# Kernel optimization log

Hardware: AMD Instinct MI355X
Metric: run time of the kernel (lower is better)

The kernel has to match this reference:

```python
import jax, jax.numpy as jnp
import numpy as np

STRIDE = 4
VOX = float(STRIDE + 1)  # voxel_size = [stride+1, stride+1]
IMG_W, IMG_H = 640.0, 480.0
N, F, E, FE, B = 300000, 64, 2400000, 8, 8


def setup_inputs() -> dict:
    key = jax.random.key(0)
    ks = jax.random.split(key, 6)
    x = jax.random.normal(ks[0], (N, F), jnp.float32)
    t = jax.random.uniform(ks[1], (N, 1), jnp.float32) * 100.0
    xy = jax.random.uniform(ks[2], (N, 2), jnp.float32) * jnp.array([IMG_W, IMG_H], jnp.float32)
    pos = jnp.concatenate([t, xy], axis=1)  # [N,3] = (time, x, y)
    batch = jnp.sort(jax.random.randint(ks[3], (N,), 0, B, jnp.int32))
    edge_index = jax.random.randint(ks[4], (2, E), 0, N, jnp.int32)
    edge_attr = jax.random.normal(ks[5], (E, FE), jnp.float32)
    return {"x": x, "pos": pos, "batch": batch, "edge_index": edge_index, "edge_attr": edge_attr}


def _forward(x, pos, batch, edge_index, edge_attr):
    n = x.shape[0]
    e = edge_index.shape[1]
    # ---- voxel_grid on pos[:,1:3] with per-sample batch separation ----
    p = pos[:, 1:3]
    start = jnp.min(p, axis=0)
    end = jnp.max(p, axis=0)
    coords = jnp.floor((p - start) / VOX).astype(jnp.int32)            # [N,2]
    dims = (jnp.floor((end - start) / VOX) + 1.0).astype(jnp.int32)    # [2]
    raw = batch * (dims[0] * dims[1]) + coords[:, 0] * dims[1] + coords[:, 1]
    # ---- consecutive_cluster: relabel voxel ids to 0..C-1 ----
    fill = jnp.iinfo(jnp.int32).max
    uniq, cluster = jnp.unique(raw, return_inverse=True, size=n, fill_value=fill)
    n_clusters = jnp.sum(uniq != fill)
    # ---- node pooling: scatter-max x, scatter-mean pos, batch per cluster ----
    new_x = jax.ops.segment_max(x, cluster, num_segments=n)
    cnt = jax.ops.segment_sum(jnp.ones((n,), pos.dtype), cluster, num_segments=n)
    new_pos = jax.ops.segment_sum(pos, cluster, num_segments=n) / jnp.maximum(cnt, 1.0)[:, None]
    new_batch = jax.ops.segment_max(batch, cluster, num_segments=n)
    valid = jnp.arange(n) < n_clusters
    new_x = jnp.where(valid[:, None], new_x, 0.0)
    new_pos = jnp.where(valid[:, None], new_pos, 0.0)
    new_batch = jnp.where(valid, new_batch, -1)
    # pos[:,1:3] //= scale (float floor-division, as torch // on float tensors)
    new_pos = new_pos.at[:, 1:3].set(jnp.floor(new_pos[:, 1:3] / float(STRIDE)))
    # ---- pool_edge: remap to cluster ids, drop self-loops, coalesce (sum attr) ----
    cs = cluster[edge_index[0]]
    cd = cluster[edge_index[1]]
    loop = cs == cd
    cs = jnp.where(loop, n, cs)   # sentinel group for self-loops (sorts last)
    cd = jnp.where(loop, n, cd)
    order = jnp.lexsort((cd, cs))
    cs_s, cd_s, ea_s = cs[order], cd[order], edge_attr[order]
    newg = jnp.concatenate([jnp.ones((1,), bool), (cs_s[1:] != cs_s[:-1]) | (cd_s[1:] != cd_s[:-1])])
    gid = jnp.cumsum(newg.astype(jnp.int32)) - 1
    src = jax.ops.segment_max(cs_s, gid, num_segments=e)
    dst = jax.ops.segment_max(cd_s, gid, num_segments=e)
    new_ea = jax.ops.segment_sum(ea_s, gid, num_segments=e)
    evalid = (jnp.arange(e) <= gid[-1]) & (src >= 0) & (src < n)
    new_edge_index = jnp.stack([jnp.where(evalid, src, -1), jnp.where(evalid, dst, -1)])
    new_ea = jnp.where(evalid[:, None], new_ea, 0.0)
    return new_x, new_pos, new_batch, new_edge_index, new_ea


def reference(x, pos, batch, edge_index, edge_attr):
    return _forward(x, pos, batch, edge_index, edge_attr)
```

## Files before the change

kernel.cpp:

```cpp
#include <hip/hip_runtime.h>

#define NN 300000
#define FF 64
#define EE 2400000
#define FEA 8
#define RAWCAP 131072
#define NCS 131072
#define NBUCK 2048
#define NSB 512
#define TILE ((EE + NSB - 1) / NSB)
#define CAP 4096

typedef unsigned long long ull;

__device__ __forceinline__ unsigned fenc(float f) {
  unsigned b = __float_as_uint(f);
  return (b & 0x80000000u) ? ~b : (b | 0x80000000u);
}
__device__ __forceinline__ float fdec(unsigned e) {
  unsigned b = (e & 0x80000000u) ? (e ^ 0x80000000u) : ~e;
  return __uint_as_float(b);
}

__global__ void init_hdr_k(unsigned* hdr) {
  if (threadIdx.x == 0) {
    hdr[0] = 0xFFFFFFFFu; hdr[1] = 0xFFFFFFFFu;
    hdr[2] = 0u;          hdr[3] = 0u;
  }
}

__global__ void minmax_k(const float* __restrict__ pos, unsigned* hdr) {
  __shared__ unsigned red[4][4];
  int t = blockIdx.x * blockDim.x + threadIdx.x;
  float mnx = 1e30f, mny = 1e30f, mxx = -1e30f, mxy = -1e30f;
  for (int i = t; i < NN; i += gridDim.x * blockDim.x) {
    float px = pos[i * 3 + 1], py = pos[i * 3 + 2];
    mnx = fminf(mnx, px); mny = fminf(mny, py);
    mxx = fmaxf(mxx, px); mxy = fmaxf(mxy, py);
  }
  for (int o = 1; o < 64; o <<= 1) {
    mnx = fminf(mnx, __shfl_xor(mnx, o));
    mny = fminf(mny, __shfl_xor(mny, o));
    mxx = fmaxf(mxx, __shfl_xor(mxx, o));
    mxy = fmaxf(mxy, __shfl_xor(mxy, o));
  }
  int wid = threadIdx.x >> 6;
  if ((threadIdx.x & 63) == 0) {
    red[wid][0] = fenc(mnx); red[wid][1] = fenc(mny);
    red[wid][2] = fenc(mxx); red[wid][3] = fenc(mxy);
  }
  __syncthreads();
  if (threadIdx.x == 0) {
    unsigned a0 = red[0][0], a1 = red[0][1], a2 = red[0][2], a3 = red[0][3];
    for (int k = 1; k < 4; k++) {
      a0 = min(a0, red[k][0]); a1 = min(a1, red[k][1]);
      a2 = max(a2, red[k][2]); a3 = max(a3, red[k][3]);
    }
    atomicMin(&hdr[0], a0); atomicMin(&hdr[1], a1);
    atomicMax(&hdr[2], a2); atomicMax(&hdr[3], a3);
  }
}

__global__ void dims_k(unsigned* hdr) {
  if (threadIdx.x == 0 && blockIdx.x == 0) {
    float mnx = fdec(hdr[0]), mny = fdec(hdr[1]);
    float mxx = fdec(hdr[2]), mxy = fdec(hdr[3]);
    int d0 = (int)(floorf((mxx - mnx) / 5.0f) + 1.0f);
    int d1 = (int)(floorf((mxy - mny) / 5.0f) + 1.0f);
    hdr[4] = (unsigned)d0;
    hdr[5] = (unsigned)d1;
    ((float*)hdr)[6] = mnx;
    ((float*)hdr)[7] = mny;
  }
}

__global__ void raw_k(const float* __restrict__ pos, const int* __restrict__ batch,
                      const unsigned* __restrict__ hdr, int* __restrict__ cluster,
                      unsigned* __restrict__ flags) {
  int i = blockIdx.x * blockDim.x + threadIdx.x;
  if (i >= NN) return;
  float mnx = ((const float*)hdr)[6], mny = ((const float*)hdr)[7];
  int d0 = (int)hdr[4], d1 = (int)hdr[5];
  int c0 = (int)floorf((pos[i * 3 + 1] - mnx) / 5.0f);
  int c1 = (int)floorf((pos[i * 3 + 2] - mny) / 5.0f);
  int raw = batch[i] * (d0 * d1) + c0 * d1 + c1;
  cluster[i] = raw;
  flags[raw] = 1u;
}

__global__ void __launch_bounds__(256)
scan_lb_k(const unsigned* __restrict__ in, unsigned* __restrict__ out, int ntot,
          unsigned* __restrict__ total_out, ull* __restrict__ desc, int nb) {
  __shared__ unsigned sc[256];
  __shared__ unsigned s_pref;
  int bid = blockIdx.x;
  int base = bid * 1024 + threadIdx.x * 4;
  unsigned v[4]; unsigned s = 0;
#pragma unroll
  for (int k = 0; k < 4; k++) {
    int i = base + k;
    v[k] = (i < ntot) ? in[i] : 0u;
    s += v[k];
  }
  sc[threadIdx.x] = s;
  __syncthreads();
  unsigned xv = s;
  for (int o = 1; o < 256; o <<= 1) {
    unsigned y = (threadIdx.x >= o) ? sc[threadIdx.x - o] : 0u;
    __syncthreads();
    xv += y;
    sc[threadIdx.x] = xv;
    __syncthreads();
  }
  unsigned btot = sc[255];
  if (threadIdx.x == 0) {
    unsigned ex = 0;
    if (bid == 0) {
      atomicExch(&desc[0], (2ULL << 32) | (ull)btot);
    } else {
      atomicExch(&desc[bid], (1ULL << 32) | (ull)btot);
      int p = bid - 1;
      while (true) {
        ull d = atomicAdd(&desc[p], 0ULL);
        unsigned fl = (unsigned)(d >> 32);
        if (fl == 2u) { ex += (unsigned)d; break; }
        if (fl == 1u) { ex += (unsigned)d; --p; }
      }
      atomicExch(&desc[bid], (2ULL << 32) | (ull)(ex + btot));
    }
    s_pref = ex;
    if (total_out && bid == nb - 1) *total_out = ex + btot;
  }
  __syncthreads();
  unsigned run = s_pref + xv - s;
#pragma unroll
  for (int k = 0; k < 4; k++) {
    int i = base + k;
    if (i < ntot) out[i] = run;
    run += v[k];
  }
}

__global__ void node_cnt_k(const unsigned* __restrict__ rank, int* __restrict__ cluster,
                           unsigned* __restrict__ cnt) {
  int i = blockIdx.x * blockDim.x + threadIdx.x;
  if (i >= NN) return;
  unsigned cl = rank[cluster[i]];
  unsigned r = atomicAdd(&cnt[cl], 1u);
  cluster[i] = (int)((r << 17) | cl);
}

__global__ void node_scatter_k(const int* __restrict__ cluster,
                               const unsigned* __restrict__ node_off,
                               int* __restrict__ nlist) {
  int i = blockIdx.x * blockDim.x + threadIdx.x;
  if (i >= NN) return;
  unsigned c = (unsigned)cluster[i];
  nlist[node_off[c & 0x1FFFFu] + (c >> 17)] = i;
}

__global__ void __launch_bounds__(256)
cluster_reduce_k(const float* __restrict__ x, const float* __restrict__ pos,
                 const int* __restrict__ batch, const int* __restrict__ nlist,
                 const unsigned* __restrict__ node_off, const unsigned* __restrict__ hdr,
                 float* __restrict__ out_x, float* __restrict__ out_pos,
                 float* __restrict__ out_batch) {
  int w = (blockIdx.x * blockDim.x + threadIdx.x) >> 6;
  int nw = (gridDim.x * blockDim.x) >> 6;
  int f = threadIdx.x & 63;
  int ncl = (int)hdr[8];
  for (int c = w; c < ncl; c += nw) {
    unsigned o0 = node_off[c];
    int len = (int)(node_off[c + 1] - o0);
    float mx = -1e38f;
    long long ps = 0;
    for (int m = 0; m < len; m++) {
      int nd = nlist[o0 + m];
      mx = fmaxf(mx, x[(size_t)nd * FF + f]);
      if (f < 3) ps += (long long)llrintf(pos[nd * 3 + f] * 65536.0f);
    }
    out_x[(size_t)c * FF + f] = mx;
    if (f < 3) {
      float v = (float)((double)ps / 65536.0 / (double)len);
      if (f > 0) v = floorf(v / 4.0f);
      out_pos[c * 3 + f] = v;
    }
    if (f == 63) out_batch[c] = (float)batch[nlist[o0]];
  }
}

__global__ void node_tail_k(const unsigned* __restrict__ hdr,
                            float* __restrict__ out_x, float* __restrict__ out_pos,
                            float* __restrict__ out_batch) {
  int ncl = (int)hdr[8];
  int total = (NN - ncl) * FF;
  for (int i = blockIdx.x * blockDim.x + threadIdx.x; i < total;
       i += gridDim.x * blockDim.x) {
    int r = ncl + (i >> 6), f = i & 63;
    out_x[(size_t)r * FF + f] = 0.0f;
    if (f < 3) out_pos[r * 3 + f] = 0.0f;
    if (f == 0) out_batch[r] = -1.0f;
  }
}


__global__ void __launch_bounds__(256)
coarse_cnt_k(const int* __restrict__ ei, const int* __restrict__ cluster,
             unsigned* __restrict__ mat) {
  __shared__ unsigned h[NBUCK];
  for (int i = threadIdx.x; i < NBUCK; i += 256) h[i] = 0u;
  __syncthreads();
  int t0 = blockIdx.x * TILE;
  for (int k = threadIdx.x; k < TILE; k += 256) {
    int t = t0 + k;
    if (t >= EE) break;
    unsigned s = (unsigned)cluster[ei[t]] & 0x1FFFFu;
    unsigned d = (unsigned)cluster[ei[EE + t]] & 0x1FFFFu;
    if (s != d) atomicAdd(&h[s >> 6], 1u);
  }
  __syncthreads();
  for (int i = threadIdx.x; i < NBUCK; i += 256)
    mat[(size_t)blockIdx.x * NBUCK + i] = h[i];
}

__global__ void transpose_k(const unsigned* __restrict__ mat, unsigned* __restrict__ matT) {
  int f = blockIdx.x * blockDim.x + threadIdx.x;
  if (f >= NSB * NBUCK) return;
  int cb = f / NSB, blk = f - cb * NSB;
  matT[f] = mat[(size_t)blk * NBUCK + cb];
}

__global__ void __launch_bounds__(256)
coarse_scatter_k(const int* __restrict__ ei, const int* __restrict__ cluster,
                 const unsigned* __restrict__ matT, ull* __restrict__ keys) {
  __shared__ unsigned cur[NBUCK];
  for (int i = threadIdx.x; i < NBUCK; i += 256)
    cur[i] = matT[(size_t)i * NSB + blockIdx.x];
  __syncthreads();
  int t0 = blockIdx.x * TILE;
  for (int k = threadIdx.x; k < TILE; k += 256) {
    int t = t0 + k;
    if (t >= EE) break;
    unsigned s = (unsigned)cluster[ei[t]] & 0x1FFFFu;
    unsigned d = (unsigned)cluster[ei[EE + t]] & 0x1FFFFu;
    if (s == d) continue;
    unsigned p = atomicAdd(&cur[s >> 6], 1u);
    keys[p] = ((ull)(s & 63u) << 39) | ((ull)d << 22) | (unsigned)t;
  }
}

__global__ void __launch_bounds__(256)
grp_emit_k(const ull* __restrict__ keys, const unsigned* __restrict__ matT,
           unsigned* __restrict__ hdr, ull* __restrict__ desc,
           const float* __restrict__ ea,
           float* __restrict__ out_src, float* __restrict__ out_dst,
           float* __restrict__ out_ea) {
  __shared__ ull sk2[CAP];
  __shared__ unsigned char hflag[CAP];
  __shared__ unsigned h[64], pre[65], cur[64], hc[64], hpre[64];
  __shared__ unsigned sG, sBase, sCnt;
  int cb = blockIdx.x;
  int tid = threadIdx.x;
  unsigned start = matT[(size_t)cb * NSB];
  unsigned end = (cb == NBUCK - 1) ? hdr[11] : matT[(size_t)(cb + 1) * NSB];
  int len = (int)(end - start);
  bool lds = (len <= CAP);
  unsigned G = 0;

  if (len > 0 && lds) {
    if (tid < 64) h[tid] = 0u;
    __syncthreads();
    for (int i = tid; i < len; i += 256)
      atomicAdd(&h[(unsigned)(keys[start + i] >> 39) & 63u], 1u);
    __syncthreads();
    if (tid == 0) {
      unsigned run = 0;
      for (int j = 0; j < 64; j++) { pre[j] = run; run += h[j]; }
      pre[64] = run;
    }
    __syncthreads();
    if (tid < 64) cur[tid] = pre[tid];
    __syncthreads();
    for (int i = tid; i < len; i += 256) {
      ull v = keys[start + i];
      unsigned j = (unsigned)(v >> 39) & 63u;
      sk2[atomicAdd(&cur[j], 1u)] = v;
    }
    __syncthreads();
    for (int i = tid; i < len; i += 256) {
      ull v = sk2[i];
      unsigned j = (unsigned)(v >> 39) & 63u;
      unsigned key23 = (unsigned)(v >> 22);
      bool head = true;
      for (int q = (int)pre[j]; q < i; ++q)
        if ((unsigned)(sk2[q] >> 22) == key23) { head = false; break; }
      hflag[i] = head ? 1 : 0;
    }
    __syncthreads();
    if (tid < 64) {
      unsigned c = 0;
      for (unsigned q = pre[tid]; q < pre[tid + 1]; ++q) c += hflag[q];
      hc[tid] = c;
    }
    __syncthreads();
    if (tid == 0) {
      unsigned run = 0;
      for (int j = 0; j < 64; j++) { hpre[j] = run; run += hc[j]; }
      sG = run;
    }
    __syncthreads();
    G = sG;
  } else if (len > 0) {
    if (tid == 0) sG = 0;
    __syncthreads();
    for (int j = 0; j < 64; j++) {
      if (tid == 0) sCnt = 0;
      __syncthreads();
      for (int i = tid; i < len; i += 256) {
        ull v = keys[start + i];
        if (((unsigned)(v >> 39) & 63u) == (unsigned)j) {
          unsigned p = atomicAdd(&sCnt, 1u);
          if (p < CAP) sk2[p] = v;
        }
      }
      __syncthreads();
      int sl = min((int)sCnt, CAP);
      for (int i = tid; i < sl; i += 256) {
        unsigned key23 = (unsigned)(sk2[i] >> 22);
        bool head = true;
        for (int q = 0; q < i; ++q)
          if ((unsigned)(sk2[q] >> 22) == key23) { head = false; break; }
        hflag[i] = head ? 1 : 0;
      }
      __syncthreads();
      if (tid == 0) {
        unsigned c = 0;
        for (int q = 0; q < sl; ++q) c += hflag[q];
        hc[j] = c; hpre[j] = sG; sG += c;
      }
      __syncthreads();
    }
    G = sG;
  }

  if (tid == 0) {
    unsigned ex = 0;
    if (cb == 0) {
      atomicExch(&desc[0], (2ULL << 32) | (ull)G);
    } else {
      atomicExch(&desc[cb], (1ULL << 32) | (ull)G);
      int p = cb - 1;
      while (true) {
        ull d = atomicAdd(&desc[p], 0ULL);
        unsigned fl = (unsigned)(d >> 32);
        if (fl == 2u) { ex += (unsigned)d; break; }
        if (fl == 1u) { ex += (unsigned)d; --p; }
      }
      atomicExch(&desc[cb], (2ULL << 32) | (ull)(ex + G));
    }
    sBase = ex;
    if (cb == NBUCK - 1) hdr[12] = ex + G;
  }
  __syncthreads();
  unsigned base = sBase;
  if (len <= 0) return;

  if (lds) {
    for (int i = tid; i < len; i += 256) {
      if (!hflag[i]) continue;
      ull v = sk2[i];
      unsigned j = (unsigned)(v >> 39) & 63u;
      unsigned key23 = (unsigned)(v >> 22);
      unsigned r = 0;
      for (unsigned q = pre[j]; q < pre[j + 1]; ++q)
        if (hflag[q] && (unsigned)(sk2[q] >> 22) < key23) r++;
      unsigned eid = (unsigned)(v & 0x3FFFFFULL);
      const float4* p4 = (const float4*)&ea[(size_t)eid * FEA];
      float4 a0 = p4[0], a1 = p4[1];
      bool single = (hc[j] == pre[j + 1] - pre[j]);
      if (!single) {
        for (unsigned q = pre[j]; q < pre[j + 1]; ++q) {
          if (q == (unsigned)i) continue;
          ull v2 = sk2[q];
          if ((unsigned)(v2 >> 22) == key23) {
            const float4* q4 = (const float4*)&ea[(size_t)(v2 & 0x3FFFFFULL) * FEA];
            float4 b0 = q4[0], b1 = q4[1];
            a0.x += b0.x; a0.y += b0.y; a0.z += b0.z; a0.w += b0.w;
            a1.x += b1.x; a1.y += b1.y; a1.z += b1.z; a1.w += b1.w;
          }
        }
      }
      unsigned row = base + hpre[j] + r;
      out_src[row] = (float)(cb * 64 + (int)j);
      out_dst[row] = (float)(key23 & 0x1FFFFu);
      float4* o = (float4*)&out_ea[(size_t)row * FEA];
      o[0] = a0; o[1] = a1;
    }
  } else {
    for (int j = 0; j < 64; j++) {
      if (tid == 0) sCnt = 0;
      __syncthreads();
      for (int i = tid; i < len; i += 256) {
        ull v = keys[start + i];
        if (((unsigned)(v >> 39) & 63u) == (unsigned)j) {
          unsigned p = atomicAdd(&sCnt, 1u);
          if (p < CAP) sk2[p] = v;
        }
      }
      __syncthreads();
      int sl = min((int)sCnt, CAP);
      for (int i = tid; i < sl; i += 256) {
        unsigned key23 = (unsigned)(sk2[i] >> 22);
        bool head = true;
        for (int q = 0; q < i; ++q)
          if ((unsigned)(sk2[q] >> 22) == key23) { head = false; break; }
        hflag[i] = head ? 1 : 0;
      }
      __syncthreads();
      for (int i = tid; i < sl; i += 256) {
        if (!hflag[i]) continue;
        ull v = sk2[i];
        unsigned key23 = (unsigned)(v >> 22);
        unsigned r = 0;
        for (int q = 0; q < sl; ++q)
          if (hflag[q] && (unsigned)(sk2[q] >> 22) < key23) r++;
        const float4* p4 = (const float4*)&ea[(size_t)(v & 0x3FFFFFULL) * FEA];
        float4 a0 = p4[0], a1 = p4[1];
        bool single = (hc[j] == (unsigned)sl);
        if (!single) {
          for (int q = 0; q < sl; ++q) {
            if (q == i) continue;
            ull v2 = sk2[q];
            if ((unsigned)(v2 >> 22) == key23) {
              const float4* q4 = (const float4*)&ea[(size_t)(v2 & 0x3FFFFFULL) * FEA];
              float4 b0 = q4[0], b1 = q4[1];
              a0.x += b0.x; a0.y += b0.y; a0.z += b0.z; a0.w += b0.w;
              a1.x += b1.x; a1.y += b1.y; a1.z += b1.z; a1.w += b1.w;
            }
          }
        }
        unsigned row = base + hpre[j] + r;
        out_src[row] = (float)(cb * 64 + j);
        out_dst[row] = (float)(key23 & 0x1FFFFu);
        float4* o = (float4*)&out_ea[(size_t)row * FEA];
        o[0] = a0; o[1] = a1;
      }
      __syncthreads();
    }
  }
}

__global__ void tail_fill_k(const unsigned* __restrict__ hdr,
                            float* __restrict__ out_src, float* __restrict__ out_dst,
                            float* __restrict__ out_ea) {
  int T = (int)hdr[12];
  for (int t = T + blockIdx.x * blockDim.x + threadIdx.x; t < EE;
       t += gridDim.x * blockDim.x) {
    out_src[t] = -1.0f;
    out_dst[t] = -1.0f;
    float4 z = make_float4(0.f, 0.f, 0.f, 0.f);
    float4* o = (float4*)&out_ea[(size_t)t * FEA];
    o[0] = z; o[1] = z;
  }
}

extern "C" void kernel_launch(void* const* d_in, const int* in_sizes, int n_in,
                              void* d_out, int out_size, void* d_ws, size_t ws_size,
                              hipStream_t stream) {
  const float* x   = (const float*)d_in[0];
  const float* pos = (const float*)d_in[1];
  const int* batch = (const int*)d_in[2];
  const int* ei    = (const int*)d_in[3];
  const float* ea  = (const float*)d_in[4];
  float* out = (float*)d_out;

  const size_t OX = 0;
  const size_t OP = (size_t)NN * FF;
  const size_t OB = OP + (size_t)NN * 3;
  const size_t OE = OB + (size_t)NN;
  const size_t OA = OE + (size_t)2 * EE;

  char* w = (char*)d_ws;
  size_t woff = 0;
  auto alloc = [&](size_t bytes) -> void* {
    void* p = w + woff;
    woff += (bytes + 255) & ~(size_t)255;
    return p;
  };
  unsigned* rank    = (unsigned*)alloc((size_t)RAWCAP * 4);
  unsigned* cnt     = (unsigned*)alloc((size_t)(NN + 1) * 4);
  ull* desc0        = (ull*)alloc(2048 * 8);
  ull* desc1        = (ull*)alloc(2048 * 8);
  ull* desc2        = (ull*)alloc(2048 * 8);
  ull* desc3        = (ull*)alloc(2048 * 8);
  size_t zero_bytes = woff;
  int* cluster      = (int*)alloc((size_t)NN * 4);
  int* nlist        = (int*)alloc((size_t)NN * 4);
  unsigned* node_off= (unsigned*)alloc((size_t)(NN + 2) * 4);
  unsigned* mat     = (unsigned*)alloc((size_t)NSB * NBUCK * 4);
  unsigned* matT    = (unsigned*)alloc((size_t)NSB * NBUCK * 4);
  unsigned* hdr     = (unsigned*)alloc(256);
  ull* keys         = (ull*)alloc((size_t)EE * 8);

  hipMemsetAsync(d_ws, 0, zero_bytes, stream);

  init_hdr_k<<<1, 64, 0, stream>>>(hdr);
  minmax_k<<<128, 256, 0, stream>>>(pos, hdr);
  dims_k<<<1, 64, 0, stream>>>(hdr);
  raw_k<<<(NN + 255) / 256, 256, 0, stream>>>(pos, batch, hdr, cluster, rank);

  auto scan1 = [&](const unsigned* in_, unsigned* out_, int ntot,
                   unsigned* total_out, ull* d_) {
    int nb = (ntot + 1023) / 1024;
    scan_lb_k<<<nb, 256, 0, stream>>>(in_, out_, ntot, total_out, d_, nb);
  };
  scan1(rank, rank, RAWCAP, hdr + 8, desc0);

  node_cnt_k<<<(NN + 255) / 256, 256, 0, stream>>>(rank, cluster, cnt);
  scan1(cnt, node_off, NN + 1, nullptr, desc1);
  node_scatter_k<<<(NN + 255) / 256, 256, 0, stream>>>(cluster, node_off, nlist);
  cluster_reduce_k<<<2048, 256, 0, stream>>>(x, pos, batch, nlist, node_off, hdr,
                                             out + OX, out + OP, out + OB);
  node_tail_k<<<2048, 256, 0, stream>>>(hdr, out + OX, out + OP, out + OB);

  coarse_cnt_k<<<NSB, 256, 0, stream>>>(ei, cluster, mat);
  transpose_k<<<(NSB * NBUCK + 255) / 256, 256, 0, stream>>>(mat, matT);
  scan1(matT, matT, NSB * NBUCK, hdr + 11, desc2);
  coarse_scatter_k<<<NSB, 256, 0, stream>>>(ei, cluster, matT, keys);
  grp_emit_k<<<NBUCK, 256, 0, stream>>>(keys, matT, hdr, desc3, ea,
                                        out + OE, out + OE + EE, out + OA);
  tail_fill_k<<<512, 256, 0, stream>>>(hdr, out + OE, out + OE + EE, out + OA);
}
```

Measured before the change: 451.8 us.

## Halve coarse edge bucket width and order grp_emit blocks by atomic ticket

Result: no change. 452.7 us (+0.2%).

```diff
diff --git a/kernel.cpp b/kernel.cpp
--- a/kernel.cpp
+++ b/kernel.cpp
@@ -5,11 +5,11 @@
 #define EE 2400000
 #define FEA 8
 #define RAWCAP 131072
-#define NCS 131072
-#define NBUCK 2048
+#define NBUCK 4096
+#define SUBB 32
 #define NSB 512
 #define TILE ((EE + NSB - 1) / NSB)
-#define CAP 4096
+#define CAP 2048
 
 typedef unsigned long long ull;
 
@@ -26,6 +26,7 @@
   if (threadIdx.x == 0) {
     hdr[0] = 0xFFFFFFFFu; hdr[1] = 0xFFFFFFFFu;
     hdr[2] = 0u;          hdr[3] = 0u;
+    hdr[13] = 0u;
   }
 }
 
@@ -216,7 +217,7 @@
     if (t >= EE) break;
     unsigned s = (unsigned)cluster[ei[t]] & 0x1FFFFu;
     unsigned d = (unsigned)cluster[ei[EE + t]] & 0x1FFFFu;
-    if (s != d) atomicAdd(&h[s >> 6], 1u);
+    if (s != d) atomicAdd(&h[s >> 5], 1u);
   }
   __syncthreads();
   for (int i = threadIdx.x; i < NBUCK; i += 256)
@@ -244,8 +245,8 @@
     unsigned s = (unsigned)cluster[ei[t]] & 0x1FFFFu;
     unsigned d = (unsigned)cluster[ei[EE + t]] & 0x1FFFFu;
     if (s == d) continue;
-    unsigned p = atomicAdd(&cur[s >> 6], 1u);
-    keys[p] = ((ull)(s & 63u) << 39) | ((ull)d << 22) | (unsigned)t;
+    unsigned p = atomicAdd(&cur[s >> 5], 1u);
+    keys[p] = ((ull)(s & 31u) << 39) | ((ull)d << 22) | (unsigned)t;
   }
 }
 
@@ -257,10 +258,12 @@
            float* __restrict__ out_ea) {
   __shared__ ull sk2[CAP];
   __shared__ unsigned char hflag[CAP];
-  __shared__ unsigned h[64], pre[65], cur[64], hc[64], hpre[64];
-  __shared__ unsigned sG, sBase, sCnt;
-  int cb = blockIdx.x;
+  __shared__ unsigned h[SUBB], pre[SUBB + 1], cur[SUBB], hc[SUBB], hpre[SUBB];
+  __shared__ unsigned sG, sBase, sCnt, sBid;
   int tid = threadIdx.x;
+  if (tid == 0) sBid = atomicAdd(&hdr[13], 1u);
+  __syncthreads();
+  int cb = (int)sBid;
   unsigned start = matT[(size_t)cb * NSB];
   unsigned end = (cb == NBUCK - 1) ? hdr[11] : matT[(size_t)(cb + 1) * NSB];
   int len = (int)(end - start);
@@ -268,36 +271,36 @@
   unsigned G = 0;
 
   if (len > 0 && lds) {
-    if (tid < 64) h[tid] = 0u;
+    if (tid < SUBB) h[tid] = 0u;
     __syncthreads();
     for (int i = tid; i < len; i += 256)
-      atomicAdd(&h[(unsigned)(keys[start + i] >> 39) & 63u], 1u);
+      atomicAdd(&h[(unsigned)(keys[start + i] >> 39) & (SUBB - 1u)], 1u);
     __syncthreads();
     if (tid == 0) {
       unsigned run = 0;
-      for (int j = 0; j < 64; j++) { pre[j] = run; run += h[j]; }
-      pre[64] = run;
-    }
-    __syncthreads();
-    if (tid < 64) cur[tid] = pre[tid];
+      for (int j = 0; j < SUBB; j++) { pre[j] = run; run += h[j]; }
+      pre[SUBB] = run;
+    }
+    __syncthreads();
+    if (tid < SUBB) cur[tid] = pre[tid];
     __syncthreads();
     for (int i = tid; i < len; i += 256) {
       ull v = keys[start + i];
-      unsigned j = (unsigned)(v >> 39) & 63u;
+      unsigned j = (unsigned)(v >> 39) & (SUBB - 1u);
       sk2[atomicAdd(&cur[j], 1u)] = v;
     }
     __syncthreads();
     for (int i = tid; i < len; i += 256) {
       ull v = sk2[i];
-      unsigned j = (unsigned)(v >> 39) & 63u;
-      unsigned key23 = (unsigned)(v >> 22);
+      unsigned j = (unsigned)(v >> 39) & (SUBB - 1u);
+      unsigned key22 = (unsigned)(v >> 22);
       bool head = true;
       for (int q = (int)pre[j]; q < i; ++q)
-        if ((unsigned)(sk2[q] >> 22) == key23) { head = false; break; }
+        if ((unsigned)(sk2[q] >> 22) == key22) { head = false; break; }
       hflag[i] = head ? 1 : 0;
     }
     __syncthreads();
-    if (tid < 64) {
+    if (tid < SUBB) {
       unsigned c = 0;
       for (unsigned q = pre[tid]; q < pre[tid + 1]; ++q) c += hflag[q];
       hc[tid] = c;
@@ -305,7 +308,7 @@
     __syncthreads();
     if (tid == 0) {
       unsigned run = 0;
-      for (int j = 0; j < 64; j++) { hpre[j] = run; run += hc[j]; }
+      for (int j = 0; j < SUBB; j++) { hpre[j] = run; run += hc[j]; }
       sG = run;
     }
     __syncthreads();
@@ -313,12 +316,12 @@
   } else if (len > 0) {
     if (tid == 0) sG = 0;
     __syncthreads();
-    for (int j = 0; j < 64; j++) {
+    for (int j = 0; j < SUBB; j++) {
       if (tid == 0) sCnt = 0;
       __syncthreads();
       for (int i = tid; i < len; i += 256) {
         ull v = keys[start + i];
-        if (((unsigned)(v >> 39) & 63u) == (unsigned)j) {
+        if (((unsigned)(v >> 39) & (SUBB - 1u)) == (unsigned)j) {
           unsigned p = atomicAdd(&sCnt, 1u);
           if (p < CAP) sk2[p] = v;
         }
@@ -326,10 +329,10 @@
       __syncthreads();
       int sl = min((int)sCnt, CAP);
       for (int i = tid; i < sl; i += 256) {
-        unsigned key23 = (unsigned)(sk2[i] >> 22);
+        unsigned key22 = (unsigned)(sk2[i] >> 22);
         bool head = true;
         for (int q = 0; q < i; ++q)
-          if ((unsigned)(sk2[q] >> 22) == key23) { head = false; break; }
+          if ((unsigned)(sk2[q] >> 22) == key22) { head = false; break; }
         hflag[i] = head ? 1 : 0;
       }
       __syncthreads();
@@ -369,11 +372,11 @@
     for (int i = tid; i < len; i += 256) {
       if (!hflag[i]) continue;
       ull v = sk2[i];
-      unsigned j = (unsigned)(v >> 39) & 63u;
-      unsigned key23 = (unsigned)(v >> 22);
+      unsigned j = (unsigned)(v >> 39) & (SUBB - 1u);
+      unsigned key22 = (unsigned)(v >> 22);
       unsigned r = 0;
       for (unsigned q = pre[j]; q < pre[j + 1]; ++q)
-        if (hflag[q] && (unsigned)(sk2[q] >> 22) < key23) r++;
+        if (hflag[q] && (unsigned)(sk2[q] >> 22) < key22) r++;
       unsigned eid = (unsigned)(v & 0x3FFFFFULL);
       const float4* p4 = (const float4*)&ea[(size_t)eid * FEA];
       float4 a0 = p4[0], a1 = p4[1];
@@ -382,7 +385,7 @@
         for (unsigned q = pre[j]; q < pre[j + 1]; ++q) {
           if (q == (unsigned)i) continue;
           ull v2 = sk2[q];
-          if ((unsigned)(v2 >> 22) == key23) {
+          if ((unsigned)(v2 >> 22) == key22) {
             const float4* q4 = (const float4*)&ea[(size_t)(v2 & 0x3FFFFFULL) * FEA];
             float4 b0 = q4[0], b1 = q4[1];
             a0.x += b0.x; a0.y += b0.y; a0.z += b0.z; a0.w += b0.w;
@@ -391,18 +394,18 @@
         }
       }
       unsigned row = base + hpre[j] + r;
-      out_src[row] = (float)(cb * 64 + (int)j);
-      out_dst[row] = (float)(key23 & 0x1FFFFu);
+      out_src[row] = (float)(cb * SUBB + (int)j);
+      out_dst[row] = (float)(key22 & 0x1FFFFu);
       float4* o = (float4*)&out_ea[(size_t)row * FEA];
       o[0] = a0; o[1] = a1;
     }
   } else {
-    for (int j = 0; j < 64; j++) {
+    for (int j = 0; j < SUBB; j++) {
       if (tid == 0) sCnt = 0;
       __syncthreads();
       for (int i = tid; i < len; i += 256) {
         ull v = keys[start + i];
-        if (((unsigned)(v >> 39) & 63u) == (unsigned)j) {
+        if (((unsigned)(v >> 39) & (SUBB - 1u)) == (unsigned)j) {
           unsigned p = atomicAdd(&sCnt, 1u);
           if (p < CAP) sk2[p] = v;
         }
@@ -410,20 +413,20 @@
       __syncthreads();
       int sl = min((int)sCnt, CAP);
       for (int i = tid; i < sl; i += 256) {
-        unsigned key23 = (unsigned)(sk2[i] >> 22);
+        unsigned key22 = (unsigned)(sk2[i] >> 22);
         bool head = true;
         for (int q = 0; q < i; ++q)
-          if ((unsigned)(sk2[q] >> 22) == key23) { head = false; break; }
+          if ((unsigned)(sk2[q] >> 22) == key22) { head = false; break; }
         hflag[i] = head ? 1 : 0;
       }
       __syncthreads();
       for (int i = tid; i < sl; i += 256) {
         if (!hflag[i]) continue;
         ull v = sk2[i];
-        unsigned key23 = (unsigned)(v >> 22);
+        unsigned key22 = (unsigned)(v >> 22);
         unsigned r = 0;
         for (int q = 0; q < sl; ++q)
-          if (hflag[q] && (unsigned)(sk2[q] >> 22) < key23) r++;
+          if (hflag[q] && (unsigned)(sk2[q] >> 22) < key22) r++;
         const float4* p4 = (const float4*)&ea[(size_t)(v & 0x3FFFFFULL) * FEA];
         float4 a0 = p4[0], a1 = p4[1];
         bool single = (hc[j] == (unsigned)sl);
@@ -431,7 +434,7 @@
           for (int q = 0; q < sl; ++q) {
             if (q == i) continue;
             ull v2 = sk2[q];
-            if ((unsigned)(v2 >> 22) == key23) {
+            if ((unsigned)(v2 >> 22) == key22) {
               const float4* q4 = (const float4*)&ea[(size_t)(v2 & 0x3FFFFFULL) * FEA];
               float4 b0 = q4[0], b1 = q4[1];
               a0.x += b0.x; a0.y += b0.y; a0.z += b0.z; a0.w += b0.w;
@@ -440,8 +443,8 @@
           }
         }
         unsigned row = base + hpre[j] + r;
-        out_src[row] = (float)(cb * 64 + j);
-        out_dst[row] = (float)(key23 & 0x1FFFFu);
+        out_src[row] = (float)(cb * SUBB + j);
+        out_dst[row] = (float)(key22 & 0x1FFFFu);
         float4* o = (float4*)&out_ea[(size_t)row * FEA];
         o[0] = a0; o[1] = a1;
       }
@@ -489,10 +492,10 @@
   };
   unsigned* rank    = (unsigned*)alloc((size_t)RAWCAP * 4);
   unsigned* cnt     = (unsigned*)alloc((size_t)(NN + 1) * 4);
-  ull* desc0        = (ull*)alloc(2048 * 8);
-  ull* desc1        = (ull*)alloc(2048 * 8);
-  ull* desc2        = (ull*)alloc(2048 * 8);
-  ull* desc3        = (ull*)alloc(2048 * 8);
+  ull* desc0        = (ull*)alloc(4096 * 8);
+  ull* desc1        = (ull*)alloc(4096 * 8);
+  ull* desc2        = (ull*)alloc(4096 * 8);
+  ull* desc3        = (ull*)alloc(4096 * 8);
   size_t zero_bytes = woff;
   int* cluster      = (int*)alloc((size_t)NN * 4);
   int* nlist        = (int*)alloc((size_t)NN * 4);
```
